# Optimization experiments

Hardware: AMD Instinct MI355X
Metric: run time of the kernel (lower is better)

## Reference

```python
import jax, jax.numpy as jnp
import numpy as np

NUM_HEADS = 8
LN_EPS = 1e-8


def setup_inputs() -> dict:
    key = jax.random.key(0)
    ks = jax.random.split(key, 10)
    B, Sq, Sk, D, U = 8, 1024, 1024, 512, 512
    s = 1.0 / np.sqrt(D)
    return {
        "queries": jax.random.normal(ks[0], (B, Sq, D), jnp.float32),
        "keys": jax.random.normal(ks[1], (B, Sk, D), jnp.float32),
        "Wq": jax.random.normal(ks[2], (D, U), jnp.float32) * s,
        "bq": jnp.zeros((U,), jnp.float32),
        "Wk": jax.random.normal(ks[3], (D, U), jnp.float32) * s,
        "bk": jnp.zeros((U,), jnp.float32),
        "Wv": jax.random.normal(ks[4], (D, U), jnp.float32) * s,
        "bv": jnp.zeros((U,), jnp.float32),
        "gamma": jnp.ones((U,), jnp.float32),
        "beta": jnp.zeros((U,), jnp.float32),
    }


def reference(queries, keys, Wq, bq, Wk, bk, Wv, bv, gamma, beta):
    H = NUM_HEADS
    B, Sq, _ = queries.shape
    Sk = keys.shape[1]
    U = Wq.shape[1]
    Dh = U // H

    # ReLU-activated Q/K/V projections
    Q = jax.nn.relu(queries @ Wq + bq)   # [B,Sq,U]
    K = jax.nn.relu(keys @ Wk + bk)      # [B,Sk,U]
    V = jax.nn.relu(keys @ Wv + bv)      # [B,Sk,U]

    # split_heads: concat(split(x, H, -1), 0) == head-major [H,B,S,Dh]
    Qh = Q.reshape(B, Sq, H, Dh).transpose(2, 0, 1, 3)
    Kh = K.reshape(B, Sk, H, Dh).transpose(2, 0, 1, 3)
    Vh = V.reshape(B, Sk, H, Dh).transpose(2, 0, 1, 3)

    scores = jnp.einsum('hbqd,hbkd->hbqk', Qh, Kh) / jnp.sqrt(
        jnp.asarray(Dh, scores_dtype := Qh.dtype))
    attn = jax.nn.softmax(scores, axis=-1)

    # post-softmax query mask: zero rows where sum(|q|)==0 ([B,Sq,1] bcast)
    qmask = (jnp.sum(jnp.abs(queries), axis=-1, keepdims=True) > 0)
    attn = attn * qmask.astype(attn.dtype)[None]  # [1,B,Sq,1] -> [H,B,Sq,Sk]

    out = jnp.einsum('hbqk,hbkd->hbqd', attn, Vh)  # [H,B,Sq,Dh]
    # merge_heads: inverse of split_heads
    out = out.transpose(1, 2, 0, 3).reshape(B, Sq, U)

    out = out + queries  # residual

    # LayerNorm over last axis (keras default), eps=1e-8
    mu = jnp.mean(out, axis=-1, keepdims=True)
    var = jnp.mean(jnp.square(out - mu), axis=-1, keepdims=True)
    return gamma * (out - mu) * jax.lax.rsqrt(var + LN_EPS) + beta
```

## Files before the change

kernel.cpp:

```cpp
#include <hip/hip_runtime.h>
#include <stdint.h>

#define ROWS 8192
#define UDIM 512
#define SEQ  1024
#define NH   8
#define DH   64
#define SCALE 0.125f
#define LOG2E 1.44269504f
#define SC_Q (SCALE * LOG2E)

typedef unsigned short u16;
typedef __bf16 bf16_t;
typedef bf16_t bf16x8 __attribute__((ext_vector_type(8)));
typedef float f32x4 __attribute__((ext_vector_type(4)));

__device__ __forceinline__ u16 f2bf(float f) {
    union { float f; uint32_t u; } v; v.f = f;
    uint32_t r = v.u + 0x7FFFu + ((v.u >> 16) & 1u);
    return (u16)(r >> 16);
}

__device__ __forceinline__ uint32_t pk_bf16(float a, float b) {
#if __has_builtin(__builtin_amdgcn_cvt_pk_bf16_f32)
    typedef __bf16 bf16x2_t __attribute__((ext_vector_type(2)));
    bf16x2_t r = __builtin_amdgcn_cvt_pk_bf16_f32(a, b);
    union { bf16x2_t v; uint32_t u; } c; c.v = r;
    return c.u;
#else
    return (uint32_t)f2bf(a) | ((uint32_t)f2bf(b) << 16);
#endif
}

__device__ __forceinline__ void async_ld16(u16* lds, const u16* g) {
    __builtin_amdgcn_global_load_lds((const __attribute__((address_space(1))) void*)g,
                                     (__attribute__((address_space(3))) void*)lds, 16, 0, 0);
}

__global__ void convqk_kernel(const float* __restrict__ q, const float* __restrict__ k,
                              u16* __restrict__ qb, u16* __restrict__ kb) {
    int w = threadIdx.x >> 6, lane = threadIdx.x & 63;
    int row = blockIdx.x * 4 + w;
    const float* src = (blockIdx.y == 0) ? q : k;
    u16* dst = (blockIdx.y == 0) ? qb : kb;
    const float4* s4 = (const float4*)(src + (size_t)row * UDIM);
    ushort4* o4 = (ushort4*)(dst + (size_t)row * UDIM);
    for (int j = 0; j < 2; j++) {
        float4 v = s4[j * 64 + lane];
        ushort4 b;
        b.x = f2bf(v.x); b.y = f2bf(v.y); b.z = f2bf(v.z); b.w = f2bf(v.w);
        o4[j * 64 + lane] = b;
    }
}

__global__ void transposeW_kernel(const float* __restrict__ Wq, const float* __restrict__ Wk,
                                  const float* __restrict__ Wv, u16* __restrict__ Wqt,
                                  u16* __restrict__ Wkt, u16* __restrict__ Wvt) {
    const float* in = (blockIdx.z == 0) ? Wq : (blockIdx.z == 1) ? Wk : Wv;
    u16* out = (blockIdx.z == 0) ? Wqt : (blockIdx.z == 1) ? Wkt : Wvt;
    __shared__ float tile[32][33];
    int k0 = blockIdx.y * 32, n0 = blockIdx.x * 32;
    int tx = threadIdx.x & 31, ty = threadIdx.x >> 5;
    for (int r = ty; r < 32; r += 8)
        tile[r][tx] = in[(size_t)(k0 + r) * UDIM + n0 + tx];
    __syncthreads();
    for (int r = ty; r < 32; r += 8)
        out[(size_t)(n0 + r) * UDIM + k0 + tx] = f2bf(tile[tx][r]);
}

#define CPAD 136
__global__ __launch_bounds__(256, 3) void proj_kernel(
    const u16* __restrict__ qb, const u16* __restrict__ kb,
    const u16* __restrict__ Wqt, const u16* __restrict__ Wkt, const u16* __restrict__ Wvt,
    const float* __restrict__ bq, const float* __restrict__ bk, const float* __restrict__ bv,
    u16* __restrict__ Qp, u16* __restrict__ Kp, u16* __restrict__ Vtp)
{
    const int z = blockIdx.z;
    const u16* A = (z == 0) ? qb : kb;
    const u16* W = (z == 0) ? Wqt : (z == 1) ? Wkt : Wvt;
    const float* bias = (z == 0) ? bq : (z == 1) ? bk : bv;

    __shared__ u16 smem[128 * CPAD];
    u16* a_s = smem;
    u16* b_s = smem + 4096;
    u16* c_s = smem;

    const int t = threadIdx.x;
    const int lane = t & 63, w = t >> 6;
    const int quad = lane >> 4, l15 = lane & 15;
    const int m0 = blockIdx.x * 128;
    const int n0 = blockIdx.y * 128;

    const int r0 = t >> 2;
    const int s0 = ((t & 3) ^ ((r0 >> 1) & 3)) * 8;
    const u16* Ag0 = &A[(size_t)(m0 + r0) * 512 + s0];
    const u16* Ag1 = Ag0 + (size_t)64 * 512;
    const u16* Wg0 = &W[(size_t)(n0 + r0) * 512 + s0];
    const u16* Wg1 = Wg0 + (size_t)64 * 512;
    u16* al0 = &a_s[t * 8];       u16* al1 = &a_s[(t + 256) * 8];
    u16* bl0 = &b_s[t * 8];       u16* bl1 = &b_s[(t + 256) * 8];

    int aoff[2], boff[8];
    for (int mi = 0; mi < 2; mi++) {
        int row = w * 32 + mi * 16 + l15;
        aoff[mi] = row * 32 + (quad ^ ((row >> 1) & 3)) * 8;
    }
    for (int ni = 0; ni < 8; ni++) {
        int row = ni * 16 + l15;
        boff[ni] = row * 32 + (quad ^ ((row >> 1) & 3)) * 8;
    }

    f32x4 acc[2][8];
    for (int mi = 0; mi < 2; mi++)
        for (int ni = 0; ni < 8; ni++)
            acc[mi][ni] = (f32x4){0.f, 0.f, 0.f, 0.f};

    for (int kt = 0; kt < 512; kt += 32) {
        async_ld16(al0, Ag0);  async_ld16(al1, Ag1);
        async_ld16(bl0, Wg0);  async_ld16(bl1, Wg1);
        Ag0 += 32; Ag1 += 32; Wg0 += 32; Wg1 += 32;
        __syncthreads();
        bf16x8 af[2], bf[8];
        for (int mi = 0; mi < 2; mi++) af[mi] = *(const bf16x8*)&a_s[aoff[mi]];
        for (int ni = 0; ni < 8; ni++) bf[ni] = *(const bf16x8*)&b_s[boff[ni]];
        for (int mi = 0; mi < 2; mi++)
            for (int ni = 0; ni < 8; ni++)
                acc[mi][ni] = __builtin_amdgcn_mfma_f32_16x16x32_bf16(af[mi], bf[ni], acc[mi][ni], 0, 0, 0);
        __syncthreads();
    }

    const float qscale = (z == 0) ? SC_Q : 1.f;
    float bvl[8];
    for (int ni = 0; ni < 8; ni++) bvl[ni] = bias[n0 + ni * 16 + l15];
    for (int mi = 0; mi < 2; mi++)
        for (int ni = 0; ni < 8; ni++)
            for (int r = 0; r < 4; r++)
                acc[mi][ni][r] = fmaxf(acc[mi][ni][r] + bvl[ni], 0.f) * qscale;

    if (z < 2) {
        for (int mi = 0; mi < 2; mi++)
            for (int ni = 0; ni < 8; ni++)
                for (int r = 0; r < 4; r++)
                    c_s[(w * 32 + mi * 16 + quad * 4 + r) * CPAD + ni * 16 + l15] =
                        f2bf(acc[mi][ni][r]);
        __syncthreads();
        u16* outp = (z == 0) ? Qp : Kp;
        for (int j = 0; j < 8; j++) {
            int c = t + j * 256;
            int mrow = c >> 4, col8 = c & 15;
            uint4 d = *(const uint4*)&c_s[mrow * CPAD + col8 * 8];
            *(uint4*)&outp[(size_t)(m0 + mrow) * 512 + n0 + col8 * 8] = d;
        }
    } else {
        for (int mi = 0; mi < 2; mi++)
            for (int ni = 0; ni < 8; ni++) {
                uint2 pk;
                pk.x = pk_bf16(acc[mi][ni][0], acc[mi][ni][1]);
                pk.y = pk_bf16(acc[mi][ni][2], acc[mi][ni][3]);
                *(uint2*)&c_s[(ni * 16 + l15) * CPAD + w * 32 + mi * 16 + quad * 4] = pk;
            }
        __syncthreads();
        const int bb = m0 >> 10, sk0 = m0 & 1023;
        for (int j = 0; j < 8; j++) {
            int c = t + j * 256;
            int nrow = c >> 4, col8 = c & 15;
            uint4 d = *(const uint4*)&c_s[nrow * CPAD + col8 * 8];
            *(uint4*)&Vtp[(size_t)(bb * 512 + n0 + nrow) * 1024 + sk0 + col8 * 8] = d;
        }
    }
}

__global__ __launch_bounds__(256, 4) void attn_kernel(
    const u16* __restrict__ Qb, const u16* __restrict__ Kb, const u16* __restrict__ Vt,
    float* __restrict__ O)
{
    __shared__ u16 q_s[64 * 64];
    __shared__ u16 k_s[64 * 64];
    __shared__ u16 v_s[64 * 64];
    __shared__ u16 p_s[64 * 64];

    const int t = threadIdx.x, lane = t & 63, w = t >> 6;
    const int quad = lane >> 4, l15 = lane & 15;
    const int fid = blockIdx.x;
    const int xcd = fid & 7, j = fid >> 3;
    const int hb = xcd * 8 + (j & 7);
    const int qt = j >> 3;
    const int h = hb & 7, b = hb >> 3;
    const int q0 = qt * 64;

    const int r0 = t >> 3;
    const int s0 = ((t & 7) ^ (r0 & 7)) * 8;
    u16* kl0 = &k_s[t * 8];       u16* kl1 = &k_s[(t + 256) * 8];
    u16* vl0 = &v_s[t * 8];       u16* vl1 = &v_s[(t + 256) * 8];
    const u16* kg0 = &Kb[(size_t)(b * 1024 + r0) * 512 + h * 64 + s0];
    const u16* kg1 = kg0 + (size_t)32 * 512;
    const u16* vg0 = &Vt[(size_t)(b * 512 + h * 64 + r0) * 1024 + s0];
    const u16* vg1 = vg0 + (size_t)32 * 1024;

    async_ld16(&q_s[t * 8],        &Qb[(size_t)(b * 1024 + q0 + r0) * 512 + h * 64 + s0]);
    async_ld16(&q_s[(t + 256) * 8], &Qb[(size_t)(b * 1024 + q0 + 32 + r0) * 512 + h * 64 + s0]);
    __syncthreads();

    const int prow = w * 16 + l15;
    bf16x8 bqf[2];
    for (int kk = 0; kk < 2; kk++)
        bqf[kk] = *(const bf16x8*)&q_s[prow * 64 + ((kk * 4 + quad) ^ (prow & 7)) * 8];

    int koff[4][2], voff[2][4], pwoff[4], proff[2];
    for (int mi = 0; mi < 4; mi++) {
        int row = mi * 16 + l15;
        koff[mi][0] = row * 64 + (quad ^ (row & 7)) * 8;
        koff[mi][1] = row * 64 + ((4 + quad) ^ (row & 7)) * 8;
        voff[0][mi] = row * 64 + (quad ^ (row & 7)) * 8;
        voff[1][mi] = row * 64 + ((4 + quad) ^ (row & 7)) * 8;
        pwoff[mi] = prow * 64 + ((mi * 2 + (quad >> 1)) ^ (prow & 7)) * 8 + (quad & 1) * 4;
    }
    for (int kk = 0; kk < 2; kk++)
        proff[kk] = prow * 64 + ((kk * 4 + quad) ^ (prow & 7)) * 8;

    float l4[4] = {0.f, 0.f, 0.f, 0.f};
    f32x4 o_acc[4];
    for (int mi = 0; mi < 4; mi++) o_acc[mi] = (f32x4){0.f, 0.f, 0.f, 0.f};

    for (int it = 0; it < 16; it++) {
        async_ld16(kl0, kg0);  async_ld16(kl1, kg1);
        async_ld16(vl0, vg0);  async_ld16(vl1, vg1);
        kg0 += (size_t)64 * 512; kg1 += (size_t)64 * 512;
        vg0 += 64; vg1 += 64;
        __syncthreads();

        f32x4 st[4];
        for (int mi = 0; mi < 4; mi++) {
            bf16x8 ak0 = *(const bf16x8*)&k_s[koff[mi][0]];
            bf16x8 ak1 = *(const bf16x8*)&k_s[koff[mi][1]];
            f32x4 a = (f32x4){0.f, 0.f, 0.f, 0.f};
            a = __builtin_amdgcn_mfma_f32_16x16x32_bf16(ak0, bqf[0], a, 0, 0, 0);
            a = __builtin_amdgcn_mfma_f32_16x16x32_bf16(ak1, bqf[1], a, 0, 0, 0);
            st[mi] = a;
        }

        for (int mi = 0; mi < 4; mi++) {
            float p0 = exp2f(st[mi][0]);
            float p1 = exp2f(st[mi][1]);
            float p2 = exp2f(st[mi][2]);
            float p3 = exp2f(st[mi][3]);
            l4[mi] += (p0 + p1) + (p2 + p3);
            uint2 pk;
            pk.x = pk_bf16(p0, p1);
            pk.y = pk_bf16(p2, p3);
            *(uint2*)&p_s[pwoff[mi]] = pk;
        }

        for (int kk = 0; kk < 2; kk++) {
            bf16x8 bp = *(const bf16x8*)&p_s[proff[kk]];
            for (int mi = 0; mi < 4; mi++) {
                bf16x8 av = *(const bf16x8*)&v_s[voff[kk][mi]];
                o_acc[mi] = __builtin_amdgcn_mfma_f32_16x16x32_bf16(av, bp, o_acc[mi], 0, 0, 0);
            }
        }
        __syncthreads();
    }

    float l = (l4[0] + l4[1]) + (l4[2] + l4[3]);
    l += __shfl_xor(l, 16, 64);
    l += __shfl_xor(l, 32, 64);
    float inv = 1.f / l;

    int gq = q0 + prow;
    for (int mi = 0; mi < 4; mi++) {
        float4 o;
        o.x = o_acc[mi][0] * inv;
        o.y = o_acc[mi][1] * inv;
        o.z = o_acc[mi][2] * inv;
        o.w = o_acc[mi][3] * inv;
        *(float4*)&O[(size_t)(b * 1024 + gq) * 512 + h * 64 + mi * 16 + quad * 4] = o;
    }
}

__global__ void ln_kernel(const float* __restrict__ O, const float* __restrict__ q,
                          const float* __restrict__ gamma, const float* __restrict__ beta,
                          float* __restrict__ out)
{
    int w = threadIdx.x >> 6, lane = threadIdx.x & 63;
    int row = blockIdx.x * 4 + w;
    const float4* O4 = (const float4*)(O + (size_t)row * UDIM);
    const float4* q4 = (const float4*)(q + (size_t)row * UDIM);
    float4* o4 = (float4*)(out + (size_t)row * UDIM);

    float4 qq[2], oo[2];
    float am = 0.f;
    for (int j = 0; j < 2; j++) {
        qq[j] = q4[j * 64 + lane];
        oo[j] = O4[j * 64 + lane];
        am += fabsf(qq[j].x) + fabsf(qq[j].y) + fabsf(qq[j].z) + fabsf(qq[j].w);
    }
    for (int off = 32; off; off >>= 1) am += __shfl_xor(am, off, 64);
    float mask = (am > 0.f) ? 1.f : 0.f;

    float4 x[2];
    float s = 0.f, ss = 0.f;
    for (int j = 0; j < 2; j++) {
        float4 v;
        v.x = oo[j].x * mask + qq[j].x;
        v.y = oo[j].y * mask + qq[j].y;
        v.z = oo[j].z * mask + qq[j].z;
        v.w = oo[j].w * mask + qq[j].w;
        x[j] = v;
        s += v.x + v.y + v.z + v.w;
        ss += v.x * v.x + v.y * v.y + v.z * v.z + v.w * v.w;
    }
    for (int off = 32; off; off >>= 1) {
        s += __shfl_xor(s, off, 64);
        ss += __shfl_xor(ss, off, 64);
    }
    float mu = s * (1.f / 512.f);
    float var = ss * (1.f / 512.f) - mu * mu;
    float rs = rsqrtf(var + 1e-8f);
    for (int j = 0; j < 2; j++) {
        float4 g = ((const float4*)gamma)[j * 64 + lane];
        float4 bb = ((const float4*)beta)[j * 64 + lane];
        float4 v;
        v.x = g.x * (x[j].x - mu) * rs + bb.x;
        v.y = g.y * (x[j].y - mu) * rs + bb.y;
        v.z = g.z * (x[j].z - mu) * rs + bb.z;
        v.w = g.w * (x[j].w - mu) * rs + bb.w;
        o4[j * 64 + lane] = v;
    }
}

extern "C" void kernel_launch(void* const* d_in, const int* in_sizes, int n_in,
                              void* d_out, int out_size, void* d_ws, size_t ws_size,
                              hipStream_t stream)
{
    const float* queries = (const float*)d_in[0];
    const float* keys    = (const float*)d_in[1];
    const float* Wq      = (const float*)d_in[2];
    const float* bq      = (const float*)d_in[3];
    const float* Wk      = (const float*)d_in[4];
    const float* bk      = (const float*)d_in[5];
    const float* Wv      = (const float*)d_in[6];
    const float* bv      = (const float*)d_in[7];
    const float* gamma   = (const float*)d_in[8];
    const float* beta    = (const float*)d_in[9];
    float* out = (float*)d_out;

    char* ws = (char*)d_ws;
    size_t off = 0;
    auto alloc = [&](size_t bytes) {
        void* p = ws + off;
        off += (bytes + 255) & ~(size_t)255;
        return p;
    };
    u16* qb   = (u16*)alloc((size_t)ROWS * UDIM * 2);
    u16* kb   = (u16*)alloc((size_t)ROWS * UDIM * 2);
    u16* Wqt  = (u16*)alloc((size_t)UDIM * UDIM * 2);
    u16* Wkt  = (u16*)alloc((size_t)UDIM * UDIM * 2);
    u16* Wvt  = (u16*)alloc((size_t)UDIM * UDIM * 2);
    u16* Qp   = (u16*)alloc((size_t)ROWS * UDIM * 2);
    u16* Kp   = (u16*)alloc((size_t)ROWS * UDIM * 2);
    u16* Vtp  = (u16*)alloc((size_t)ROWS * UDIM * 2);
    float* Of = (float*)alloc((size_t)ROWS * UDIM * 4);

    convqk_kernel<<<dim3(ROWS / 4, 2), 256, 0, stream>>>(queries, keys, qb, kb);
    transposeW_kernel<<<dim3(16, 16, 3), 256, 0, stream>>>(Wq, Wk, Wv, Wqt, Wkt, Wvt);
    proj_kernel<<<dim3(64, 4, 3), 256, 0, stream>>>(qb, kb, Wqt, Wkt, Wvt, bq, bk, bv, Qp, Kp, Vtp);
    attn_kernel<<<1024, 256, 0, stream>>>(Qp, Kp, Vtp, Of);
    ln_kernel<<<ROWS / 4, 256, 0, stream>>>(Of, queries, gamma, beta, out);
}
```

Before: 161.8 us.

## Process 128 queries per attention block to reuse K/V tiles

The attention kernel now handles two 64-row query subtiles per block, so each K/V tile loaded into LDS, and the fragments read from it into registers, serve twice as many queries. The grid is halved and the launch-bounds occupancy hint drops from 4 to 3 blocks per CU. The loop-end barrier becomes a mid-iteration barrier, since V fragments are held in registers before the P·V step. This trades more registers, more LDS and fewer blocks for less K/V global and LDS traffic per query.

```diff
diff --git a/kernel.cpp b/kernel.cpp
--- a/kernel.cpp
+++ b/kernel.cpp
@@ -170,14 +170,14 @@
     }
 }
 
-__global__ __launch_bounds__(256, 4) void attn_kernel(
+__global__ __launch_bounds__(256, 3) void attn_kernel(
     const u16* __restrict__ Qb, const u16* __restrict__ Kb, const u16* __restrict__ Vt,
     float* __restrict__ O)
 {
-    __shared__ u16 q_s[64 * 64];
+    __shared__ u16 q_s[128 * 64];
     __shared__ u16 k_s[64 * 64];
     __shared__ u16 v_s[64 * 64];
-    __shared__ u16 p_s[64 * 64];
+    __shared__ u16 p_s[128 * 64];
 
     const int t = threadIdx.x, lane = t & 63, w = t >> 6;
     const int quad = lane >> 4, l15 = lane & 15;
@@ -186,7 +186,7 @@
     const int hb = xcd * 8 + (j & 7);
     const int qt = j >> 3;
     const int h = hb & 7, b = hb >> 3;
-    const int q0 = qt * 64;
+    const int q0 = qt * 128;
 
     const int r0 = t >> 3;
     const int s0 = ((t & 7) ^ (r0 & 7)) * 8;
@@ -197,30 +197,40 @@
     const u16* vg0 = &Vt[(size_t)(b * 512 + h * 64 + r0) * 1024 + s0];
     const u16* vg1 = vg0 + (size_t)32 * 1024;
 
-    async_ld16(&q_s[t * 8],        &Qb[(size_t)(b * 1024 + q0 + r0) * 512 + h * 64 + s0]);
-    async_ld16(&q_s[(t + 256) * 8], &Qb[(size_t)(b * 1024 + q0 + 32 + r0) * 512 + h * 64 + s0]);
+    for (int rnd = 0; rnd < 4; rnd++) {
+        int c = t + rnd * 256;
+        int row = c >> 3;
+        int jg = (c & 7) ^ (row & 7);
+        async_ld16(&q_s[c * 8], &Qb[(size_t)(b * 1024 + q0 + row) * 512 + h * 64 + jg * 8]);
+    }
     __syncthreads();
 
-    const int prow = w * 16 + l15;
-    bf16x8 bqf[2];
-    for (int kk = 0; kk < 2; kk++)
-        bqf[kk] = *(const bf16x8*)&q_s[prow * 64 + ((kk * 4 + quad) ^ (prow & 7)) * 8];
-
-    int koff[4][2], voff[2][4], pwoff[4], proff[2];
+    const int prow0 = w * 16 + l15;
+    bf16x8 bqf[2][2];
+    for (int s = 0; s < 2; s++) {
+        int row = s * 64 + prow0;
+        for (int kk = 0; kk < 2; kk++)
+            bqf[s][kk] = *(const bf16x8*)&q_s[row * 64 + ((kk * 4 + quad) ^ (row & 7)) * 8];
+    }
+
+    int koff[4][2], pwoff[2][4], proff[2][2];
     for (int mi = 0; mi < 4; mi++) {
         int row = mi * 16 + l15;
         koff[mi][0] = row * 64 + (quad ^ (row & 7)) * 8;
         koff[mi][1] = row * 64 + ((4 + quad) ^ (row & 7)) * 8;
-        voff[0][mi] = row * 64 + (quad ^ (row & 7)) * 8;
-        voff[1][mi] = row * 64 + ((4 + quad) ^ (row & 7)) * 8;
-        pwoff[mi] = prow * 64 + ((mi * 2 + (quad >> 1)) ^ (prow & 7)) * 8 + (quad & 1) * 4;
-    }
-    for (int kk = 0; kk < 2; kk++)
-        proff[kk] = prow * 64 + ((kk * 4 + quad) ^ (prow & 7)) * 8;
-
-    float l4[4] = {0.f, 0.f, 0.f, 0.f};
-    f32x4 o_acc[4];
-    for (int mi = 0; mi < 4; mi++) o_acc[mi] = (f32x4){0.f, 0.f, 0.f, 0.f};
+    }
+    for (int s = 0; s < 2; s++) {
+        int row = s * 64 + prow0;
+        for (int mi = 0; mi < 4; mi++)
+            pwoff[s][mi] = row * 64 + ((mi * 2 + (quad >> 1)) ^ (row & 7)) * 8 + (quad & 1) * 4;
+        for (int kk = 0; kk < 2; kk++)
+            proff[s][kk] = row * 64 + ((kk * 4 + quad) ^ (row & 7)) * 8;
+    }
+
+    float l_lane[2] = {0.f, 0.f};
+    f32x4 o_acc[2][4];
+    for (int s = 0; s < 2; s++)
+        for (int mi = 0; mi < 4; mi++) o_acc[s][mi] = (f32x4){0.f, 0.f, 0.f, 0.f};
 
     for (int it = 0; it < 16; it++) {
         async_ld16(kl0, kg0);  async_ld16(kl1, kg1);
@@ -229,51 +239,60 @@
         vg0 += 64; vg1 += 64;
         __syncthreads();
 
-        f32x4 st[4];
+        bf16x8 ak[4][2];
         for (int mi = 0; mi < 4; mi++) {
-            bf16x8 ak0 = *(const bf16x8*)&k_s[koff[mi][0]];
-            bf16x8 ak1 = *(const bf16x8*)&k_s[koff[mi][1]];
-            f32x4 a = (f32x4){0.f, 0.f, 0.f, 0.f};
-            a = __builtin_amdgcn_mfma_f32_16x16x32_bf16(ak0, bqf[0], a, 0, 0, 0);
-            a = __builtin_amdgcn_mfma_f32_16x16x32_bf16(ak1, bqf[1], a, 0, 0, 0);
-            st[mi] = a;
-        }
-
+            ak[mi][0] = *(const bf16x8*)&k_s[koff[mi][0]];
+            ak[mi][1] = *(const bf16x8*)&k_s[koff[mi][1]];
+        }
+        bf16x8 av[2][4];
+        for (int kk = 0; kk < 2; kk++)
+            for (int mi = 0; mi < 4; mi++)
+                av[kk][mi] = *(const bf16x8*)&v_s[koff[mi][kk]];
+
+        for (int s = 0; s < 2; s++) {
+            f32x4 st[4];
+            for (int mi = 0; mi < 4; mi++) {
+                f32x4 a = (f32x4){0.f, 0.f, 0.f, 0.f};
+                a = __builtin_amdgcn_mfma_f32_16x16x32_bf16(ak[mi][0], bqf[s][0], a, 0, 0, 0);
+                a = __builtin_amdgcn_mfma_f32_16x16x32_bf16(ak[mi][1], bqf[s][1], a, 0, 0, 0);
+                st[mi] = a;
+            }
+            for (int mi = 0; mi < 4; mi++) {
+                float p0 = exp2f(st[mi][0]);
+                float p1 = exp2f(st[mi][1]);
+                float p2 = exp2f(st[mi][2]);
+                float p3 = exp2f(st[mi][3]);
+                l_lane[s] += (p0 + p1) + (p2 + p3);
+                uint2 pk;
+                pk.x = pk_bf16(p0, p1);
+                pk.y = pk_bf16(p2, p3);
+                *(uint2*)&p_s[pwoff[s][mi]] = pk;
+            }
+        }
+        __syncthreads();
+
+        for (int s = 0; s < 2; s++)
+            for (int kk = 0; kk < 2; kk++) {
+                bf16x8 bp = *(const bf16x8*)&p_s[proff[s][kk]];
+                for (int mi = 0; mi < 4; mi++)
+                    o_acc[s][mi] = __builtin_amdgcn_mfma_f32_16x16x32_bf16(av[kk][mi], bp, o_acc[s][mi], 0, 0, 0);
+            }
+    }
+
+    for (int s = 0; s < 2; s++) {
+        float l = l_lane[s];
+        l += __shfl_xor(l, 16, 64);
+        l += __shfl_xor(l, 32, 64);
+        float inv = 1.f / l;
+        int gq = q0 + s * 64 + prow0;
         for (int mi = 0; mi < 4; mi++) {
-            float p0 = exp2f(st[mi][0]);
-            float p1 = exp2f(st[mi][1]);
-            float p2 = exp2f(st[mi][2]);
-            float p3 = exp2f(st[mi][3]);
-            l4[mi] += (p0 + p1) + (p2 + p3);
-            uint2 pk;
-            pk.x = pk_bf16(p0, p1);
-            pk.y = pk_bf16(p2, p3);
-            *(uint2*)&p_s[pwoff[mi]] = pk;
-        }
-
-        for (int kk = 0; kk < 2; kk++) {
-            bf16x8 bp = *(const bf16x8*)&p_s[proff[kk]];
-            for (int mi = 0; mi < 4; mi++) {
-                bf16x8 av = *(const bf16x8*)&v_s[voff[kk][mi]];
-                o_acc[mi] = __builtin_amdgcn_mfma_f32_16x16x32_bf16(av, bp, o_acc[mi], 0, 0, 0);
-            }
-        }
-        __syncthreads();
-    }
-
-    float l = (l4[0] + l4[1]) + (l4[2] + l4[3]);
-    l += __shfl_xor(l, 16, 64);
-    l += __shfl_xor(l, 32, 64);
-    float inv = 1.f / l;
-
-    int gq = q0 + prow;
-    for (int mi = 0; mi < 4; mi++) {
-        float4 o;
-        o.x = o_acc[mi][0] * inv;
-        o.y = o_acc[mi][1] * inv;
-        o.z = o_acc[mi][2] * inv;
-        o.w = o_acc[mi][3] * inv;
-        *(float4*)&O[(size_t)(b * 1024 + gq) * 512 + h * 64 + mi * 16 + quad * 4] = o;
+            float4 o;
+            o.x = o_acc[s][mi][0] * inv;
+            o.y = o_acc[s][mi][1] * inv;
+            o.z = o_acc[s][mi][2] * inv;
+            o.w = o_acc[s][mi][3] * inv;
+            *(float4*)&O[(size_t)(b * 1024 + gq) * 512 + h * 64 + mi * 16 + quad * 4] = o;
+        }
     }
 }
 
@@ -364,6 +383,6 @@
     convqk_kernel<<<dim3(ROWS / 4, 2), 256, 0, stream>>>(queries, keys, qb, kb);
     transposeW_kernel<<<dim3(16, 16, 3), 256, 0, stream>>>(Wq, Wk, Wv, Wqt, Wkt, Wvt);
     proj_kernel<<<dim3(64, 4, 3), 256, 0, stream>>>(qb, kb, Wqt, Wkt, Wvt, bq, bk, bv, Qp, Kp, Vtp);
-    attn_kernel<<<1024, 256, 0, stream>>>(Qp, Kp, Vtp, Of);
+    attn_kernel<<<512, 256, 0, stream>>>(Qp, Kp, Vtp, Of);
     ln_kernel<<<ROWS / 4, 256, 0, stream>>>(Of, queries, gamma, beta, out);
 }
```

Measured after the change: 170.1 us. +5.1%, slower.
